# Kernel tuning notes

Hardware: AMD Instinct MI355X
Metric: run time of the kernel (lower is better)

## Reference

```python
import jax, jax.numpy as jnp
import numpy as np

WINDOW = 16      # window_size[0]
LANDM_H = 8      # closest_square_factors(64) = (8, 8)
LANDM_W = 8
MAX_VAL = 5.0
PINV_ITERS = 6


def activ(x):
    # ExpLinearAfterThreshold: exp(clamp(x, max=5)) + relu(x - 5)
    return jnp.exp(jnp.minimum(x, MAX_VAL)) + jax.nn.relu(x - MAX_VAL)


def pool_landmarks(x):
    # x: [B, H, N, d] with N = WINDOW*WINDOW.
    B, H, N, d = x.shape
    kh, kw = WINDOW // LANDM_H, WINDOW // LANDM_W
    x = x.reshape(B, H, LANDM_H, kh, LANDM_W, kw, d)
    return x.mean(axis=(3, 5)).reshape(B, H, LANDM_H * LANDM_W, d)  # [B, H, L, d]


def moore_penrose_pinv(x, iters=PINV_ITERS):
    # x: [B, H, L, L]
    abs_x = jnp.abs(x)
    col = abs_x.sum(axis=-1)
    row = abs_x.sum(axis=-2)
    z = jnp.swapaxes(x, -1, -2) / (jnp.max(col) * jnp.max(row) + 1e-15)
    I = jnp.eye(x.shape[-1], dtype=x.dtype)
    for _ in range(iters):
        xz = x @ z
        z = 0.25 * z @ (13.0 * I - xz @ (15.0 * I - xz @ (7.0 * I - xz)))
    return z


def setup_inputs() -> dict:
    key = jax.random.key(0)
    kq, kk, kv = jax.random.split(key, 3)
    shape = (256, 16, 256, 64)  # [B_, num_heads, window^2, head_dim]
    q = jax.random.normal(kq, shape, dtype=jnp.float32)
    k = jax.random.normal(kk, shape, dtype=jnp.float32)
    v = jax.random.normal(kv, shape, dtype=jnp.float32)
    return {"q": q, "k": k, "v": v}


def reference(q, k, v):
    # q, k, v: [B, H, N, d]
    q_m = pool_landmarks(q)  # [B, H, L, d]
    k_m = pool_landmarks(k)  # [B, H, L, d]

    temp = activ(jnp.einsum('bhld,bhmd->bhlm', q_m, k_m))   # [B, H, L, L]
    pinv = moore_penrose_pinv(temp, PINV_ITERS)              # [B, H, L, L]

    # kernel(q_m, k) @ [v | 1]  -> [B, H, L, d+1]
    v1 = jnp.concatenate([v, jnp.ones_like(v[..., :1])], axis=-1)
    kv = jnp.einsum('bhln,bhne->bhle', activ(jnp.einsum('bhld,bhnd->bhln', q_m, k)), v1)

    # kernel(q, k_m) @ pinv @ kv  -> [B, H, N, d+1]
    qk = activ(jnp.einsum('bhnd,bhld->bhnl', q, k_m))        # [B, H, N, L]
    prod = jnp.einsum('bhnl,bhle->bhne', qk @ pinv, kv)

    return prod[..., :-1] / (prod[..., -1:] + 1e-12)
```

## Files before the change

kernel.cpp:

```cpp
#include <hip/hip_runtime.h>
#include <math.h>


#define G_TOT 4096
#define TPB_R 256
#define TPB_M 1024
typedef _Float16 f16;
typedef __attribute__((ext_vector_type(2))) _Float16 f16x2;
typedef __attribute__((ext_vector_type(4))) _Float16 f16x4;
typedef __attribute__((ext_vector_type(8))) _Float16 f16x8;
typedef __attribute__((ext_vector_type(4))) float f32x4;
typedef __attribute__((ext_vector_type(16))) float f32x16;

#define NPLANES 18
#define SMEM_BYTES (NPLANES * 4096 * 2 + 2 * 64 * 4)

#define LSCALE 2048.0f
#define LINV   (1.0f / 2048.0f)
#define ZS     1024.0f
#define ZINV   (1.0f / 1024.0f)

struct HL { f16 h, l; };
__device__ __forceinline__ HL split2(float v) {
    HL r;
    r.h = (f16)v;
    r.l = (f16)((v - (float)r.h) * LSCALE);
    return r;
}
__device__ __forceinline__ float join2(f16 h, f16 l) {
    return (float)h + (float)l * LINV;
}
__device__ __forceinline__ int swi(int r, int c) {
    return (r << 6) + (c ^ ((r & 7) << 3));
}
__device__ __forceinline__ float activ_f(float x) {
    return expf(fminf(x, 5.0f)) + fmaxf(x - 5.0f, 0.0f);
}
__device__ __forceinline__ void split_w(f16* Ph, f16* Pl, int r, int c, float v) {
    HL s = split2(v);
    const int o = swi(r, c);
    Ph[o] = s.h;
    Pl[o] = s.l;
}
__device__ __forceinline__ f16x2 mk2(f16 a, f16 b) { f16x2 r; r[0]=a; r[1]=b; return r; }
__device__ __forceinline__ f16x4 mk4(f16 a, f16 b, f16 c, f16 d) { f16x4 r; r[0]=a;r[1]=b;r[2]=c;r[3]=d; return r; }
__device__ __forceinline__ f32x4 z4() { f32x4 z = {0.f,0.f,0.f,0.f}; return z; }
__device__ __forceinline__ f32x16 z16() {
    f32x16 z;
#pragma unroll
    for (int i = 0; i < 16; ++i) z[i] = 0.f;
    return z;
}

__device__ __forceinline__ f32x4 mm16(const f16* __restrict__ Ah, const f16* __restrict__ Al,
                                      const f16* __restrict__ Bh, const f16* __restrict__ Bl,
                                      int arow, int brow, int kg, f32x4 acc) {
    const int abase = arow << 6, axor = (arow & 7) << 3;
    const int bbase = brow << 6, bxor = (brow & 7) << 3;
    f32x4 ax1 = z4(), ax2 = z4();
#pragma unroll
    for (int s = 0; s < 2; ++s) {
        const int k0 = (s << 5) + (kg << 3);
        const int ao = abase + (k0 ^ axor);
        const int bo = bbase + (k0 ^ bxor);
        f16x8 a_h = *(const f16x8*)(Ah + ao);
        f16x8 a_l = *(const f16x8*)(Al + ao);
        f16x8 b_h = *(const f16x8*)(Bh + bo);
        f16x8 b_l = *(const f16x8*)(Bl + bo);
        acc = __builtin_amdgcn_mfma_f32_16x16x32_f16(a_h, b_h, acc, 0, 0, 0);
        ax1 = __builtin_amdgcn_mfma_f32_16x16x32_f16(a_h, b_l, ax1, 0, 0, 0);
        ax2 = __builtin_amdgcn_mfma_f32_16x16x32_f16(a_l, b_h, ax2, 0, 0, 0);
    }
    acc += (ax1 + ax2) * LINV;
    return acc;
}

__device__ __forceinline__ f32x16 mm64q(const f16* __restrict__ Ah, const f16* __restrict__ Al,
                                        const f16* __restrict__ Bh, const f16* __restrict__ Bl,
                                        int lane, int wr, int wc, f32x16 acc) {
    const int cl = lane & 31, hh = lane >> 5;
    const int ar = (wr << 5) + cl, br = (wc << 5) + cl;
    const int abase = ar << 6, axor = (ar & 7) << 3;
    const int bbase = br << 6, bxor = (br & 7) << 3;
    f32x16 ax1 = z16();
    f32x16 ax2 = z16();
#pragma unroll
    for (int ks = 0; ks < 4; ++ks) {
        const int k0 = (ks << 4) + (hh << 3);
        const int ao = abase + (k0 ^ axor);
        const int bo = bbase + (k0 ^ bxor);
        f16x8 a_h = *(const f16x8*)(Ah + ao);
        f16x8 a_l = *(const f16x8*)(Al + ao);
        f16x8 b_h = *(const f16x8*)(Bh + bo);
        f16x8 b_l = *(const f16x8*)(Bl + bo);
        acc = __builtin_amdgcn_mfma_f32_32x32x16_f16(a_h, b_h, acc, 0, 0, 0);
        ax1 = __builtin_amdgcn_mfma_f32_32x32x16_f16(a_h, b_l, ax1, 0, 0, 0);
        ax2 = __builtin_amdgcn_mfma_f32_32x32x16_f16(a_l, b_h, ax2, 0, 0, 0);
    }
    acc += (ax1 + ax2) * LINV;
    return acc;
}

__device__ __forceinline__ void wr_rm(float4 vv, f16* Ph, f16* Pl, int t) {
    const int r = t >> 4, c4 = (t & 15) << 2;
    const int o = swi(r, c4);
    HL s0 = split2(vv.x), s1 = split2(vv.y), s2 = split2(vv.z), s3 = split2(vv.w);
    *(f16x4*)(Ph + o) = mk4(s0.h, s1.h, s2.h, s3.h);
    *(f16x4*)(Pl + o) = mk4(s0.l, s1.l, s2.l, s3.l);
}
__device__ __forceinline__ void ld_vt(const float* __restrict__ src, int t,
                                      float2& va, float2& vb) {
    const int n0 = (t >> 5) << 1, e0 = (t & 31) << 1;
    va = *(const float2*)(src + (size_t)n0 * 64 + e0);
    vb = *(const float2*)(src + (size_t)(n0 + 1) * 64 + e0);
}
__device__ __forceinline__ void wr_vt(float2 va, float2 vb, f16* Ph, f16* Pl, int t) {
    const int n0 = (t >> 5) << 1, e0 = (t & 31) << 1;
    HL ax = split2(va.x), ay = split2(va.y), bx = split2(vb.x), by = split2(vb.y);
    const int o0 = swi(e0, n0), o1 = swi(e0 + 1, n0);
    *(f16x2*)(Ph + o0) = mk2(ax.h, bx.h);
    *(f16x2*)(Pl + o0) = mk2(ax.l, bx.l);
    *(f16x2*)(Ph + o1) = mk2(ay.h, by.h);
    *(f16x2*)(Pl + o1) = mk2(ay.l, by.l);
}

__device__ __forceinline__ void pool_global1024(const float* __restrict__ src,
                                                f16* Ph, f16* Pl, int t) {
    const int L = t >> 4, d0 = (t & 15) << 2;
    const int nb = ((L >> 3) << 5) + ((L & 7) << 1);
    const float* p = src + (size_t)nb * 64 + d0;
    float4 a = *(const float4*)p;
    float4 b = *(const float4*)(p + 64);
    float4 c = *(const float4*)(p + 1024);
    float4 d = *(const float4*)(p + 1088);
    HL s0 = split2(0.25f * (a.x + b.x + c.x + d.x));
    HL s1 = split2(0.25f * (a.y + b.y + c.y + d.y));
    HL s2 = split2(0.25f * (a.z + b.z + c.z + d.z));
    HL s3 = split2(0.25f * (a.w + b.w + c.w + d.w));
    const int o = swi(L, d0);
    *(f16x4*)(Ph + o) = mk4(s0.h, s1.h, s2.h, s3.h);
    *(f16x4*)(Pl + o) = mk4(s0.l, s1.l, s2.l, s3.l);
}

__device__ __forceinline__ void pool_lds512(const f16* Kh, const f16* Kl,
                                            f16* Ph, f16* Pl, int t, int tt) {
    const int ll = t >> 5, d0 = (t & 31) << 1;
    const int rb = ((ll >> 3) << 5) + ((ll & 7) << 1);
    float s0 = 0.f, s1 = 0.f;
#pragma unroll
    for (int rr = 0; rr < 4; ++rr) {
        const int r = rb + (rr & 1) + ((rr >> 1) << 4);
        const int o = swi(r, d0);
        f16x2 h = *(const f16x2*)(Kh + o);
        f16x2 l = *(const f16x2*)(Kl + o);
        s0 += join2(h[0], l[0]);
        s1 += join2(h[1], l[1]);
    }
    const int L = (tt << 4) + ll;
    HL p0 = split2(0.25f * s0), p1 = split2(0.25f * s1);
    const int o = swi(L, d0);
    *(f16x2*)(Ph + o) = mk2(p0.h, p1.h);
    *(f16x2*)(Pl + o) = mk2(p0.l, p1.l);
}

__device__ __forceinline__ void pool_global_r(const float* __restrict__ src,
                                              f16* Ph, f16* Pl, int t) {
    const int ll = t >> 4, d0 = (t & 15) << 2;
    const int rb = ((ll >> 3) << 5) + ((ll & 7) << 1);
#pragma unroll
    for (int tt = 0; tt < 4; ++tt) {
        const float* p = src + (size_t)((tt << 6) + rb) * 64 + d0;
        float4 a = *(const float4*)p;
        float4 b = *(const float4*)(p + 64);
        float4 c = *(const float4*)(p + 1024);
        float4 d = *(const float4*)(p + 1088);
        const int L = (tt << 4) + ll;
        split_w(Ph, Pl, L, d0 + 0, 0.25f * (a.x + b.x + c.x + d.x));
        split_w(Ph, Pl, L, d0 + 1, 0.25f * (a.y + b.y + c.y + d.y));
        split_w(Ph, Pl, L, d0 + 2, 0.25f * (a.z + b.z + c.z + d.z));
        split_w(Ph, Pl, L, d0 + 3, 0.25f * (a.w + b.w + c.w + d.w));
    }
}

#define WAVE_SUM32(v)            \
    v += __shfl_xor(v, 1);       \
    v += __shfl_xor(v, 2);       \
    v += __shfl_xor(v, 4);       \
    v += __shfl_xor(v, 8);       \
    v += __shfl_xor(v, 16);

__global__ void k_init(float* ws) {
    if (threadIdx.x < 2) ws[threadIdx.x] = 0.0f;
}

__global__ __launch_bounds__(TPB_R) void k_reduce(const float* __restrict__ q,
                                                  const float* __restrict__ k,
                                                  float* __restrict__ ws) {
    __shared__ f16 pls[4 * 4096];
    __shared__ float rowS[64], colS[64];
    const int t = threadIdx.x, g = blockIdx.x;
    const int lane = t & 63, wv = t >> 6, wr = wv >> 1, wc = wv & 1;
    const int cl = lane & 31, hh = lane >> 5;
    if (t < 64) rowS[t] = 0.f;
    else if (t < 128) colS[t - 64] = 0.f;
    pool_global_r(q + (size_t)g * 16384, pls, pls + 4096, t);
    pool_global_r(k + (size_t)g * 16384, pls + 8192, pls + 12288, t);
    __syncthreads();
    f32x16 a = mm64q(pls, pls + 4096, pls + 8192, pls + 12288, lane, wr, wc, z16());
    float colp = 0.f;
#pragma unroll
    for (int m = 0; m < 16; ++m) {
        float x = activ_f(a[m]);
        const int R = (wr << 5) + (m & 3) + ((m >> 2) << 3) + (hh << 2);
        float vs = x;
        WAVE_SUM32(vs)
        if (cl == 0) atomicAdd(&rowS[R], vs);
        colp += x;
    }
    colp += __shfl_xor(colp, 32);
    if (hh == 0) atomicAdd(&colS[(wc << 5) + cl], colp);
    __syncthreads();
    if (t < 64) {
        float vmx = rowS[t];
        for (int off = 1; off < 64; off <<= 1) vmx = fmaxf(vmx, __shfl_xor(vmx, off));
        if (t == 0) atomicMax((int*)ws, __float_as_int(vmx));
    } else if (t < 128) {
        float vmx = colS[t - 64];
        for (int off = 1; off < 64; off <<= 1) vmx = fmaxf(vmx, __shfl_xor(vmx, off));
        if (t == 64) atomicMax(((int*)ws) + 1, __float_as_int(vmx));
    }
}

__global__ __launch_bounds__(TPB_M, 4) void k_main(const float* __restrict__ q,
                                                   const float* __restrict__ k,
                                                   const float* __restrict__ v,
                                                   const float* __restrict__ ws,
                                                   float* __restrict__ out) {
    extern __shared__ f16 smu[];
    float* kv1 = (float*)(smu + NPLANES * 4096);
    float* den = kv1 + 64;
    const int t = threadIdx.x, g = blockIdx.x;
    const int lane = t & 63, w = t >> 6;
    const int ti = w & 3, tj = w >> 2;
    const int fr = lane & 15, kg = lane >> 4;
    const int arow = (ti << 4) + fr;
    const int brow = (tj << 4) + fr;
    const int C = brow;
    const int Rb = (ti << 4) + (kg << 2);
    const float* Gq = q + (size_t)g * 16384;
    const float* Gk = k + (size_t)g * 16384;
    const float* Gv = v + (size_t)g * 16384;
    float* og = out + (size_t)g * 16384;

    f16* QMh = smu +  0 * 4096; f16* QMl = smu +  1 * 4096;
    f16* KMh = smu +  2 * 4096; f16* KMl = smu +  3 * 4096;
    f16* P4  = smu +  4 * 4096; f16* P5  = smu +  5 * 4096;
    f16* Zrh = smu +  6 * 4096; f16* Zrl = smu +  7 * 4096;
    f16* Zth = smu +  8 * 4096; f16* Ztl = smu +  9 * 4096;
    f16* PAh = smu + 10 * 4096; f16* PAl = smu + 11 * 4096;
    f16* PBh = smu + 12 * 4096; f16* PBl = smu + 13 * 4096;
    f16* KVh = smu + 14 * 4096; f16* KVl = smu + 15 * 4096;
    f16* T2h = smu + 16 * 4096; f16* T2l = smu + 17 * 4096;
    f16* oTh = QMh; f16* oTl = QMl;

    if (t < 64) kv1[t] = 0.f;
    pool_global1024(Gq, QMh, QMl, t);
    __syncthreads();

    f32x4 kva = z4();
    float4 kreg = *(const float4*)(Gk + (size_t)t * 4);
    float2 va, vb;
    ld_vt(Gv, t, va, vb);
    for (int tt = 0; tt < 4; ++tt) {
        wr_rm(kreg, P4, P5, t);
        wr_vt(va, vb, PAh, PAl, t);
        if (tt < 3) {
            kreg = *(const float4*)(Gk + (size_t)(tt + 1) * 4096 + (size_t)t * 4);
            ld_vt(Gv + (size_t)(tt + 1) * 4096, t, va, vb);
        }
        __syncthreads();
        if (t < 512) pool_lds512(P4, P5, KMh, KMl, t, tt);
        f32x4 s = mm16(QMh, QMl, P4, P5, arow, brow, kg, z4());
#pragma unroll
        for (int m = 0; m < 4; ++m) {
            const int R = Rb + m;
            const float x = activ_f(s[m]);
            split_w(PBh, PBl, R, C, x);
            float vs = x;
            vs += __shfl_xor(vs, 1); vs += __shfl_xor(vs, 2);
            vs += __shfl_xor(vs, 4); vs += __shfl_xor(vs, 8);
            if (fr == 0) atomicAdd(&kv1[R], vs);
        }
        __syncthreads();
        kva = mm16(PBh, PBl, PAh, PAl, arow, brow, kg, kva);
        __syncthreads();
    }
#pragma unroll
    for (int m = 0; m < 4; ++m) split_w(KVh, KVl, C, Rb + m, kva[m]);

    {
        f32x4 x0 = mm16(QMh, QMl, KMh, KMl, arow, brow, kg, z4());
#pragma unroll
        for (int m = 0; m < 4; ++m) split_w(P4, P5, Rb + m, C, activ_f(x0[m]));
    }
    __syncthreads();

    {
        const float scale = ZS / (ws[0] * ws[1] + 1e-15f);
        const int r0 = (t >> 5) << 1, c0 = (t & 31) << 1;
        const int o00 = swi(r0, c0), o10 = swi(r0 + 1, c0);
        const float v00 = join2(P4[o00], P5[o00]) * scale;
        const float v01 = join2(P4[o00 + 1], P5[o00 + 1]) * scale;
        const float v10 = join2(P4[o10], P5[o10]) * scale;
        const float v11 = join2(P4[o10 + 1], P5[o10 + 1]) * scale;
        HL s00 = split2(v00), s01 = split2(v01), s10 = split2(v10), s11 = split2(v11);
        *(f16x2*)(Zth + o00) = mk2(s00.h, s01.h);
        *(f16x2*)(Ztl + o00) = mk2(s00.l, s01.l);
        *(f16x2*)(Zth + o10) = mk2(s10.h, s11.h);
        *(f16x2*)(Ztl + o10) = mk2(s10.l, s11.l);
        const int p0 = swi(c0, r0), p1 = swi(c0 + 1, r0);
        *(f16x2*)(Zrh + p0) = mk2(s00.h, s10.h);
        *(f16x2*)(Zrl + p0) = mk2(s00.l, s10.l);
        *(f16x2*)(Zrh + p1) = mk2(s01.h, s11.h);
        *(f16x2*)(Zrl + p1) = mk2(s01.l, s11.l);
    }
    __syncthreads();

    for (int it = 0; it < 6; ++it) {
        f32x4 a0 = mm16(P4, P5, Zth, Ztl, arow, brow, kg, z4());
#pragma unroll
        for (int m = 0; m < 4; ++m) {
            const int R = Rb + m;
            const float t1 = a0[m] * ZINV;
            split_w(PAh, PAl, R, C, t1);
            split_w(PBh, PBl, C, R, t1);
        }
        __syncthreads();
        f32x4 b0 = mm16(PAh, PAl, PBh, PBl, arow, brow, kg, z4());
#pragma unroll
        for (int m = 0; m < 4; ++m) split_w(T2h, T2l, Rb + m, C, b0[m]);
        __syncthreads();
        f32x4 c0a = mm16(T2h, T2l, PBh, PBl, arow, brow, kg, z4());
#pragma unroll
        for (int m = 0; m < 4; ++m) {
            const int R = Rb + m;
            const int o = swi(R, C);
            const float t1 = join2(PAh[o], PAl[o]);
            const float t2 = join2(T2h[o], T2l[o]);
            const float ov = ((R == C) ? 13.f : 0.f) - 15.f * t1 + 7.f * t2 - c0a[m];
            split_w(oTh, oTl, C, R, ov);
        }
        __syncthreads();
        f32x4 d0 = mm16(Zrh, Zrl, oTh, oTl, arow, brow, kg, z4());
        __syncthreads();
#pragma unroll
        for (int m = 0; m < 4; ++m) {
            const int R = Rb + m;
            const float z0 = 0.25f * d0[m];
            split_w(Zrh, Zrl, R, C, z0);
            split_w(Zth, Ztl, C, R, z0);
        }
        __syncthreads();
    }

    const float kvC = kv1[C];
    float4 qreg = *(const float4*)(Gq + (size_t)t * 4);
    for (int tt = 0; tt < 4; ++tt) {
        if (t < 64) den[t] = 0.f;
        wr_rm(qreg, P4, P5, t);
        if (tt < 3) qreg = *(const float4*)(Gq + (size_t)(tt + 1) * 4096 + (size_t)t * 4);
        __syncthreads();
        f32x4 q0 = mm16(P4, P5, KMh, KMl, arow, brow, kg, z4());
#pragma unroll
        for (int m = 0; m < 4; ++m) split_w(PBh, PBl, Rb + m, C, activ_f(q0[m]));
        __syncthreads();
        f32x4 w0 = mm16(PBh, PBl, Zth, Ztl, arow, brow, kg, z4());
#pragma unroll
        for (int m = 0; m < 4; ++m) {
            const int R = Rb + m;
            const float wv = w0[m] * ZINV;
            split_w(PAh, PAl, R, C, wv);
            float d_ = wv * kvC;
            d_ += __shfl_xor(d_, 1); d_ += __shfl_xor(d_, 2);
            d_ += __shfl_xor(d_, 4); d_ += __shfl_xor(d_, 8);
            if (fr == 0) atomicAdd(&den[R], d_);
        }
        __syncthreads();
        f32x4 p0 = mm16(PAh, PAl, KVh, KVl, arow, brow, kg, z4());
#pragma unroll
        for (int m = 0; m < 4; ++m) {
            const int R = Rb + m;
            const float inv = 1.0f / (den[R] + 1e-12f);
            og[(size_t)((tt << 6) + R) * 64 + C] = p0[m] * inv;
        }
        __syncthreads();
    }
}

extern "C" void kernel_launch(void* const* d_in, const int* in_sizes, int n_in,
                              void* d_out, int out_size, void* d_ws, size_t ws_size,
                              hipStream_t stream) {
    const float* q = (const float*)d_in[0];
    const float* k = (const float*)d_in[1];
    const float* v = (const float*)d_in[2];
    float* out = (float*)d_out;
    float* ws  = (float*)d_ws;
    (void)in_sizes; (void)n_in; (void)out_size; (void)ws_size;

    hipFuncSetAttribute((const void*)k_main,
                        hipFuncAttributeMaxDynamicSharedMemorySize, SMEM_BYTES);

    k_init<<<1, 64, 0, stream>>>(ws);
    k_reduce<<<G_TOT, TPB_R, 0, stream>>>(q, k, ws);
    k_main<<<G_TOT, TPB_M, SMEM_BYTES, stream>>>(q, k, v, ws, out);
}
```

Baseline: 909.0 us.

## Restructure main kernel with register fragments, double buffering, and fewer barriers

Rewrites the main per-group kernel so that MFMA operand fragments are loaded once into registers (Frag) and reused, for example the QM, KM, Z and KV fragments. K/V tiles are double-buffered so the next tile's global load and LDS write overlap the current matmuls. The Newton-Schulz iterations ping-pong between Z buffers and keep t1/t2 in registers instead of rereading LDS, which cuts barriers and LDS traffic. The main kernel also switches to fast __expf and uses per-tile denominators. This trades extra register pressure and slightly lower exp accuracy for fewer synchronisations, and it cuts LDS planes from 18 to 16.

Measured after the change: 768.5 us. 1.18x faster.

```diff
diff --git a/kernel.cpp b/kernel.cpp
--- a/kernel.cpp
+++ b/kernel.cpp
@@ -12,8 +12,8 @@
 typedef __attribute__((ext_vector_type(4))) float f32x4;
 typedef __attribute__((ext_vector_type(16))) float f32x16;
 
-#define NPLANES 18
-#define SMEM_BYTES (NPLANES * 4096 * 2 + 2 * 64 * 4)
+#define NPLANES 16
+#define SMEM_BYTES (NPLANES * 4096 * 2 + 320 * 4)
 
 #define LSCALE 2048.0f
 #define LINV   (1.0f / 2048.0f)
@@ -34,6 +34,9 @@
     return (r << 6) + (c ^ ((r & 7) << 3));
 }
 __device__ __forceinline__ float activ_f(float x) {
+    return __expf(fminf(x, 5.0f)) + fmaxf(x - 5.0f, 0.0f);
+}
+__device__ __forceinline__ float activ_r(float x) {
     return expf(fminf(x, 5.0f)) + fmaxf(x - 5.0f, 0.0f);
 }
 __device__ __forceinline__ void split_w(f16* Ph, f16* Pl, int r, int c, float v) {
@@ -52,53 +55,43 @@
     return z;
 }
 
-__device__ __forceinline__ f32x4 mm16(const f16* __restrict__ Ah, const f16* __restrict__ Al,
-                                      const f16* __restrict__ Bh, const f16* __restrict__ Bl,
-                                      int arow, int brow, int kg, f32x4 acc) {
-    const int abase = arow << 6, axor = (arow & 7) << 3;
-    const int bbase = brow << 6, bxor = (brow & 7) << 3;
+struct Frag { f16x8 h[2], l[2]; };
+
+__device__ __forceinline__ Frag ld_frag(const f16* __restrict__ Ph,
+                                        const f16* __restrict__ Pl,
+                                        int row, int kg) {
+    Frag f;
+    const int base = row << 6, x = (row & 7) << 3;
+#pragma unroll
+    for (int s = 0; s < 2; ++s) {
+        const int o = base + ((((s << 5) + (kg << 3))) ^ x);
+        f.h[s] = *(const f16x8*)(Ph + o);
+        f.l[s] = *(const f16x8*)(Pl + o);
+    }
+    return f;
+}
+
+__device__ __forceinline__ f32x4 mm16_rr(const Frag& A, const Frag& B, f32x4 acc) {
     f32x4 ax1 = z4(), ax2 = z4();
 #pragma unroll
     for (int s = 0; s < 2; ++s) {
-        const int k0 = (s << 5) + (kg << 3);
-        const int ao = abase + (k0 ^ axor);
-        const int bo = bbase + (k0 ^ bxor);
-        f16x8 a_h = *(const f16x8*)(Ah + ao);
-        f16x8 a_l = *(const f16x8*)(Al + ao);
-        f16x8 b_h = *(const f16x8*)(Bh + bo);
-        f16x8 b_l = *(const f16x8*)(Bl + bo);
-        acc = __builtin_amdgcn_mfma_f32_16x16x32_f16(a_h, b_h, acc, 0, 0, 0);
-        ax1 = __builtin_amdgcn_mfma_f32_16x16x32_f16(a_h, b_l, ax1, 0, 0, 0);
-        ax2 = __builtin_amdgcn_mfma_f32_16x16x32_f16(a_l, b_h, ax2, 0, 0, 0);
+        acc = __builtin_amdgcn_mfma_f32_16x16x32_f16(A.h[s], B.h[s], acc, 0, 0, 0);
+        ax1 = __builtin_amdgcn_mfma_f32_16x16x32_f16(A.h[s], B.l[s], ax1, 0, 0, 0);
+        ax2 = __builtin_amdgcn_mfma_f32_16x16x32_f16(A.l[s], B.h[s], ax2, 0, 0, 0);
     }
     acc += (ax1 + ax2) * LINV;
     return acc;
 }
 
-__device__ __forceinline__ f32x16 mm64q(const f16* __restrict__ Ah, const f16* __restrict__ Al,
-                                        const f16* __restrict__ Bh, const f16* __restrict__ Bl,
-                                        int lane, int wr, int wc, f32x16 acc) {
-    const int cl = lane & 31, hh = lane >> 5;
-    const int ar = (wr << 5) + cl, br = (wc << 5) + cl;
-    const int abase = ar << 6, axor = (ar & 7) << 3;
-    const int bbase = br << 6, bxor = (br & 7) << 3;
-    f32x16 ax1 = z16();
-    f32x16 ax2 = z16();
-#pragma unroll
-    for (int ks = 0; ks < 4; ++ks) {
-        const int k0 = (ks << 4) + (hh << 3);
-        const int ao = abase + (k0 ^ axor);
-        const int bo = bbase + (k0 ^ bxor);
-        f16x8 a_h = *(const f16x8*)(Ah + ao);
-        f16x8 a_l = *(const f16x8*)(Al + ao);
-        f16x8 b_h = *(const f16x8*)(Bh + bo);
-        f16x8 b_l = *(const f16x8*)(Bl + bo);
-        acc = __builtin_amdgcn_mfma_f32_32x32x16_f16(a_h, b_h, acc, 0, 0, 0);
-        ax1 = __builtin_amdgcn_mfma_f32_32x32x16_f16(a_h, b_l, ax1, 0, 0, 0);
-        ax2 = __builtin_amdgcn_mfma_f32_32x32x16_f16(a_l, b_h, ax2, 0, 0, 0);
-    }
-    acc += (ax1 + ax2) * LINV;
-    return acc;
+__device__ __forceinline__ void wfrag_rm(f16* Ph, f16* Pl, int Rb, int C, const float* v) {
+#pragma unroll
+    for (int m = 0; m < 4; ++m) split_w(Ph, Pl, Rb + m, C, v[m]);
+}
+__device__ __forceinline__ void wfrag_t(f16* Ph, f16* Pl, int Rb, int C, const float* v) {
+    const int o = swi(C, Rb);
+    HL s0 = split2(v[0]), s1 = split2(v[1]), s2 = split2(v[2]), s3 = split2(v[3]);
+    *(f16x4*)(Ph + o) = mk4(s0.h, s1.h, s2.h, s3.h);
+    *(f16x4*)(Pl + o) = mk4(s0.l, s1.l, s2.l, s3.l);
 }
 
 __device__ __forceinline__ void wr_rm(float4 vv, f16* Ph, f16* Pl, int t) {
@@ -163,6 +156,31 @@
     *(f16x2*)(Pl + o) = mk2(p0.l, p1.l);
 }
 
+__device__ __forceinline__ f32x16 mm64q(const f16* __restrict__ Ah, const f16* __restrict__ Al,
+                                        const f16* __restrict__ Bh, const f16* __restrict__ Bl,
+                                        int lane, int wr, int wc, f32x16 acc) {
+    const int cl = lane & 31, hh = lane >> 5;
+    const int ar = (wr << 5) + cl, br = (wc << 5) + cl;
+    const int abase = ar << 6, axor = (ar & 7) << 3;
+    const int bbase = br << 6, bxor = (br & 7) << 3;
+    f32x16 ax1 = z16();
+    f32x16 ax2 = z16();
+#pragma unroll
+    for (int ks = 0; ks < 4; ++ks) {
+        const int k0 = (ks << 4) + (hh << 3);
+        const int ao = abase + (k0 ^ axor);
+        const int bo = bbase + (k0 ^ bxor);
+        f16x8 a_h = *(const f16x8*)(Ah + ao);
+        f16x8 a_l = *(const f16x8*)(Al + ao);
+        f16x8 b_h = *(const f16x8*)(Bh + bo);
+        f16x8 b_l = *(const f16x8*)(Bl + bo);
+        acc = __builtin_amdgcn_mfma_f32_32x32x16_f16(a_h, b_h, acc, 0, 0, 0);
+        ax1 = __builtin_amdgcn_mfma_f32_32x32x16_f16(a_h, b_l, ax1, 0, 0, 0);
+        ax2 = __builtin_amdgcn_mfma_f32_32x32x16_f16(a_l, b_h, ax2, 0, 0, 0);
+    }
+    acc += (ax1 + ax2) * LINV;
+    return acc;
+}
 __device__ __forceinline__ void pool_global_r(const float* __restrict__ src,
                                               f16* Ph, f16* Pl, int t) {
     const int ll = t >> 4, d0 = (t & 15) << 2;
@@ -210,7 +228,7 @@
     float colp = 0.f;
 #pragma unroll
     for (int m = 0; m < 16; ++m) {
-        float x = activ_f(a[m]);
+        float x = activ_r(a[m]);
         const int R = (wr << 5) + (m & 3) + ((m >> 2) << 3) + (hh << 2);
         float vs = x;
         WAVE_SUM32(vs)
@@ -252,147 +270,170 @@
     const float* Gv = v + (size_t)g * 16384;
     float* og = out + (size_t)g * 16384;
 
-    f16* QMh = smu +  0 * 4096; f16* QMl = smu +  1 * 4096;
-    f16* KMh = smu +  2 * 4096; f16* KMl = smu +  3 * 4096;
-    f16* P4  = smu +  4 * 4096; f16* P5  = smu +  5 * 4096;
-    f16* Zrh = smu +  6 * 4096; f16* Zrl = smu +  7 * 4096;
-    f16* Zth = smu +  8 * 4096; f16* Ztl = smu +  9 * 4096;
-    f16* PAh = smu + 10 * 4096; f16* PAl = smu + 11 * 4096;
-    f16* PBh = smu + 12 * 4096; f16* PBl = smu + 13 * 4096;
-    f16* KVh = smu + 14 * 4096; f16* KVl = smu + 15 * 4096;
-    f16* T2h = smu + 16 * 4096; f16* T2l = smu + 17 * 4096;
-    f16* oTh = QMh; f16* oTl = QMl;
-
-    if (t < 64) kv1[t] = 0.f;
-    pool_global1024(Gq, QMh, QMl, t);
+    f16* Xh  = smu +  0 * 4096; f16* Xl  = smu +  1 * 4096;
+    f16* SAh = smu +  2 * 4096; f16* SAl = smu +  3 * 4096;
+    f16* SBh = smu +  4 * 4096; f16* SBl = smu +  5 * 4096;
+    f16* KMh = smu +  6 * 4096; f16* KMl = smu +  7 * 4096;
+    f16* SCh = smu +  8 * 4096; f16* SCl = smu +  9 * 4096;
+    f16* KVh = smu + 10 * 4096; f16* KVl = smu + 11 * 4096;
+    f16* Z0rh= smu + 12 * 4096; f16* Z0rl= smu + 13 * 4096;
+    f16* Z0th= smu + 14 * 4096; f16* Z0tl= smu + 15 * 4096;
+
+    if (t < 320) kv1[t] = 0.f;
+    pool_global1024(Gq, Z0rh, Z0rl, t);
+    {
+        float4 kreg = *(const float4*)(Gk + (size_t)t * 4);
+        float2 va, vb; ld_vt(Gv, t, va, vb);
+        wr_rm(kreg, SAh, SAl, t);
+        wr_vt(va, vb, SBh, SBl, t);
+    }
     __syncthreads();
 
+    Frag fQM = ld_frag(Z0rh, Z0rl, arow, kg);
+
     f32x4 kva = z4();
-    float4 kreg = *(const float4*)(Gk + (size_t)t * 4);
-    float2 va, vb;
-    ld_vt(Gv, t, va, vb);
     for (int tt = 0; tt < 4; ++tt) {
-        wr_rm(kreg, P4, P5, t);
-        wr_vt(va, vb, PAh, PAl, t);
+        f16* vch = (tt & 1) ? Xh : SBh;  f16* vcl = (tt & 1) ? Xl : SBl;
+        f16* vnh = (tt & 1) ? SBh : Xh;  f16* vnl = (tt & 1) ? SBl : Xl;
+        float4 kregN; float2 vaN, vbN;
         if (tt < 3) {
-            kreg = *(const float4*)(Gk + (size_t)(tt + 1) * 4096 + (size_t)t * 4);
-            ld_vt(Gv + (size_t)(tt + 1) * 4096, t, va, vb);
-        }
-        __syncthreads();
-        if (t < 512) pool_lds512(P4, P5, KMh, KMl, t, tt);
-        f32x4 s = mm16(QMh, QMl, P4, P5, arow, brow, kg, z4());
+            kregN = *(const float4*)(Gk + (size_t)(tt + 1) * 4096 + (size_t)t * 4);
+            ld_vt(Gv + (size_t)(tt + 1) * 4096, t, vaN, vbN);
+        }
+        if (t < 512) pool_lds512(SAh, SAl, KMh, KMl, t, tt);
+        {
+            Frag bK = ld_frag(SAh, SAl, brow, kg);
+            f32x4 s = mm16_rr(fQM, bK, z4());
+            float sv[4];
+#pragma unroll
+            for (int m = 0; m < 4; ++m) {
+                sv[m] = activ_f(s[m]);
+                float vs = sv[m];
+                vs += __shfl_xor(vs, 1); vs += __shfl_xor(vs, 2);
+                vs += __shfl_xor(vs, 4); vs += __shfl_xor(vs, 8);
+                if (fr == 0) atomicAdd(&kv1[Rb + m], vs);
+            }
+            wfrag_rm(SCh, SCl, Rb, C, sv);
+        }
+        if (tt < 3) wr_vt(vaN, vbN, vnh, vnl, t);
+        __syncthreads();
+        {
+            Frag aS = ld_frag(SCh, SCl, arow, kg);
+            Frag bV = ld_frag(vch, vcl, brow, kg);
+            kva = mm16_rr(aS, bV, kva);
+        }
+        if (tt < 3) wr_rm(kregN, SAh, SAl, t);
+        __syncthreads();
+    }
+
+    {
+        float kvv[4] = {kva[0], kva[1], kva[2], kva[3]};
+        wfrag_t(KVh, KVl, Rb, C, kvv);
+        Frag fKMb = ld_frag(KMh, KMl, brow, kg);
+        f32x4 x0 = mm16_rr(fQM, fKMb, z4());
+        const float scale = ZS / (ws[0] * ws[1] + 1e-15f);
+        float xv[4], zv[4];
+#pragma unroll
+        for (int m = 0; m < 4; ++m) { xv[m] = activ_f(x0[m]); zv[m] = xv[m] * scale; }
+        wfrag_rm(Xh, Xl, Rb, C, xv);
+        wfrag_t (Z0rh, Z0rl, Rb, C, zv);
+        wfrag_rm(Z0th, Z0tl, Rb, C, zv);
+    }
+    __syncthreads();
+
+    Frag fX = ld_frag(Xh, Xl, arow, kg);
+    f16 *zrh = Z0rh, *zrl = Z0rl, *zth = Z0th, *ztl = Z0tl;
+    f16 *nrh = SAh,  *nrl = SAl,  *nth = SCh,  *ntl = SCl;
+#pragma unroll
+    for (int it = 0; it < 6; ++it) {
+        Frag bz = ld_frag(zth, ztl, brow, kg);
+        f32x4 a1 = mm16_rr(fX, bz, z4());
+        float t1k[4];
+#pragma unroll
+        for (int m = 0; m < 4; ++m) t1k[m] = a1[m] * ZINV;
+        wfrag_rm(nrh, nrl, Rb, C, t1k);
+        wfrag_t (nth, ntl, Rb, C, t1k);
+        __syncthreads();
+        Frag aT1 = ld_frag(nrh, nrl, arow, kg);
+        Frag bT1 = ld_frag(nth, ntl, brow, kg);
+        f32x4 a2 = mm16_rr(aT1, bT1, z4());
+        float t2k[4];
+#pragma unroll
+        for (int m = 0; m < 4; ++m) t2k[m] = a2[m];
+        wfrag_rm(Xh, Xl, Rb, C, t2k);
+        __syncthreads();
+        Frag aT2 = ld_frag(Xh, Xl, arow, kg);
+        f32x4 a3 = mm16_rr(aT2, bT1, z4());
+        float ov[4];
 #pragma unroll
         for (int m = 0; m < 4; ++m) {
             const int R = Rb + m;
-            const float x = activ_f(s[m]);
-            split_w(PBh, PBl, R, C, x);
-            float vs = x;
-            vs += __shfl_xor(vs, 1); vs += __shfl_xor(vs, 2);
-            vs += __shfl_xor(vs, 4); vs += __shfl_xor(vs, 8);
-            if (fr == 0) atomicAdd(&kv1[R], vs);
-        }
-        __syncthreads();
-        kva = mm16(PBh, PBl, PAh, PAl, arow, brow, kg, kva);
-        __syncthreads();
-    }
-#pragma unroll
-    for (int m = 0; m < 4; ++m) split_w(KVh, KVl, C, Rb + m, kva[m]);
-
+            ov[m] = ((R == C) ? 13.f : 0.f) - 15.f * t1k[m] + 7.f * t2k[m] - a3[m];
+        }
+        wfrag_t(SBh, SBl, Rb, C, ov);
+        __syncthreads();
+        Frag aZ = ld_frag(zrh, zrl, arow, kg);
+        Frag bO = ld_frag(SBh, SBl, brow, kg);
+        f32x4 a4 = mm16_rr(aZ, bO, z4());
+        float zk[4];
+#pragma unroll
+        for (int m = 0; m < 4; ++m) zk[m] = 0.25f * a4[m];
+        wfrag_rm(nrh, nrl, Rb, C, zk);
+        wfrag_t (nth, ntl, Rb, C, zk);
+        __syncthreads();
+        f16* tp;
+        tp = zrh; zrh = nrh; nrh = tp;  tp = zrl; zrl = nrl; nrl = tp;
+        tp = zth; zth = nth; nth = tp;  tp = ztl; ztl = ntl; ntl = tp;
+    }
+
+    Frag fKM = ld_frag(KMh, KMl, brow, kg);
+    Frag fZt = ld_frag(Z0th, Z0tl, brow, kg);
+    Frag fKV = ld_frag(KVh, KVl, brow, kg);
+    const float kvC = kv1[C];
     {
-        f32x4 x0 = mm16(QMh, QMl, KMh, KMl, arow, brow, kg, z4());
-#pragma unroll
-        for (int m = 0; m < 4; ++m) split_w(P4, P5, Rb + m, C, activ_f(x0[m]));
+        float4 qreg = *(const float4*)(Gq + (size_t)t * 4);
+        wr_rm(qreg, SAh, SAl, t);
     }
     __syncthreads();
-
-    {
-        const float scale = ZS / (ws[0] * ws[1] + 1e-15f);
-        const int r0 = (t >> 5) << 1, c0 = (t & 31) << 1;
-        const int o00 = swi(r0, c0), o10 = swi(r0 + 1, c0);
-        const float v00 = join2(P4[o00], P5[o00]) * scale;
-        const float v01 = join2(P4[o00 + 1], P5[o00 + 1]) * scale;
-        const float v10 = join2(P4[o10], P5[o10]) * scale;
-        const float v11 = join2(P4[o10 + 1], P5[o10 + 1]) * scale;
-        HL s00 = split2(v00), s01 = split2(v01), s10 = split2(v10), s11 = split2(v11);
-        *(f16x2*)(Zth + o00) = mk2(s00.h, s01.h);
-        *(f16x2*)(Ztl + o00) = mk2(s00.l, s01.l);
-        *(f16x2*)(Zth + o10) = mk2(s10.h, s11.h);
-        *(f16x2*)(Ztl + o10) = mk2(s10.l, s11.l);
-        const int p0 = swi(c0, r0), p1 = swi(c0 + 1, r0);
-        *(f16x2*)(Zrh + p0) = mk2(s00.h, s10.h);
-        *(f16x2*)(Zrl + p0) = mk2(s00.l, s10.l);
-        *(f16x2*)(Zrh + p1) = mk2(s01.h, s11.h);
-        *(f16x2*)(Zrl + p1) = mk2(s01.l, s11.l);
-    }
-    __syncthreads();
-
-    for (int it = 0; it < 6; ++it) {
-        f32x4 a0 = mm16(P4, P5, Zth, Ztl, arow, brow, kg, z4());
-#pragma unroll
-        for (int m = 0; m < 4; ++m) {
-            const int R = Rb + m;
-            const float t1 = a0[m] * ZINV;
-            split_w(PAh, PAl, R, C, t1);
-            split_w(PBh, PBl, C, R, t1);
-        }
-        __syncthreads();
-        f32x4 b0 = mm16(PAh, PAl, PBh, PBl, arow, brow, kg, z4());
-#pragma unroll
-        for (int m = 0; m < 4; ++m) split_w(T2h, T2l, Rb + m, C, b0[m]);
-        __syncthreads();
-        f32x4 c0a = mm16(T2h, T2l, PBh, PBl, arow, brow, kg, z4());
-#pragma unroll
-        for (int m = 0; m < 4; ++m) {
-            const int R = Rb + m;
-            const int o = swi(R, C);
-            const float t1 = join2(PAh[o], PAl[o]);
-            const float t2 = join2(T2h[o], T2l[o]);
-            const float ov = ((R == C) ? 13.f : 0.f) - 15.f * t1 + 7.f * t2 - c0a[m];
-            split_w(oTh, oTl, C, R, ov);
-        }
-        __syncthreads();
-        f32x4 d0 = mm16(Zrh, Zrl, oTh, oTl, arow, brow, kg, z4());
-        __syncthreads();
-#pragma unroll
-        for (int m = 0; m < 4; ++m) {
-            const int R = Rb + m;
-            const float z0 = 0.25f * d0[m];
-            split_w(Zrh, Zrl, R, C, z0);
-            split_w(Zth, Ztl, C, R, z0);
-        }
-        __syncthreads();
-    }
-
-    const float kvC = kv1[C];
-    float4 qreg = *(const float4*)(Gq + (size_t)t * 4);
     for (int tt = 0; tt < 4; ++tt) {
-        if (t < 64) den[t] = 0.f;
-        wr_rm(qreg, P4, P5, t);
-        if (tt < 3) qreg = *(const float4*)(Gq + (size_t)(tt + 1) * 4096 + (size_t)t * 4);
-        __syncthreads();
-        f32x4 q0 = mm16(P4, P5, KMh, KMl, arow, brow, kg, z4());
-#pragma unroll
-        for (int m = 0; m < 4; ++m) split_w(PBh, PBl, Rb + m, C, activ_f(q0[m]));
-        __syncthreads();
-        f32x4 w0 = mm16(PBh, PBl, Zth, Ztl, arow, brow, kg, z4());
-#pragma unroll
-        for (int m = 0; m < 4; ++m) {
-            const int R = Rb + m;
-            const float wv = w0[m] * ZINV;
-            split_w(PAh, PAl, R, C, wv);
-            float d_ = wv * kvC;
-            d_ += __shfl_xor(d_, 1); d_ += __shfl_xor(d_, 2);
-            d_ += __shfl_xor(d_, 4); d_ += __shfl_xor(d_, 8);
-            if (fr == 0) atomicAdd(&den[R], d_);
-        }
-        __syncthreads();
-        f32x4 p0 = mm16(PAh, PAl, KVh, KVl, arow, brow, kg, z4());
-#pragma unroll
-        for (int m = 0; m < 4; ++m) {
-            const int R = Rb + m;
-            const float inv = 1.0f / (den[R] + 1e-12f);
-            og[(size_t)((tt << 6) + R) * 64 + C] = p0[m] * inv;
-        }
+        float4 qregN;
+        if (tt < 3) qregN = *(const float4*)(Gq + (size_t)(tt + 1) * 4096 + (size_t)t * 4);
+        {
+            Frag aQ = ld_frag(SAh, SAl, arow, kg);
+            f32x4 q0 = mm16_rr(aQ, fKM, z4());
+            float qv[4];
+#pragma unroll
+            for (int m = 0; m < 4; ++m) qv[m] = activ_f(q0[m]);
+            wfrag_rm(SCh, SCl, Rb, C, qv);
+        }
+        __syncthreads();
+        float* dn = den + (tt << 6);
+        {
+            Frag aK = ld_frag(SCh, SCl, arow, kg);
+            f32x4 w0 = mm16_rr(aK, fZt, z4());
+            float wv[4];
+#pragma unroll
+            for (int m = 0; m < 4; ++m) {
+                wv[m] = w0[m] * ZINV;
+                float d_ = wv[m] * kvC;
+                d_ += __shfl_xor(d_, 1); d_ += __shfl_xor(d_, 2);
+                d_ += __shfl_xor(d_, 4); d_ += __shfl_xor(d_, 8);
+                if (fr == 0) atomicAdd(&dn[Rb + m], d_);
+            }
+            wfrag_rm(SBh, SBl, Rb, C, wv);
+        }
+        __syncthreads();
+        {
+            Frag aW = ld_frag(SBh, SBl, arow, kg);
+            f32x4 p0 = mm16_rr(aW, fKV, z4());
+#pragma unroll
+            for (int m = 0; m < 4; ++m) {
+                const int R = Rb + m;
+                const float inv = 1.0f / (dn[R] + 1e-12f);
+                og[(size_t)((tt << 6) + R) * 64 + C] = p0[m] * inv;
+            }
+        }
+        if (tt < 3) wr_rm(qregN, SAh, SAl, t);
         __syncthreads();
     }
 }
```
